# Optimization experiments

Measured on AMD Instinct MI355X. Metric: run time of the kernel, lower is better.

## Reference

```python
import jax, jax.numpy as jnp
import numpy as np

BS, N, H = 8, 2048, 512
NEG_INF = -1.0e9
LEAKY_SLOPE = 0.01  # torch nn.LeakyReLU default


def setup_inputs() -> dict:
    key = jax.random.key(0)
    ks = jax.random.split(key, 8)
    feats = jax.random.normal(ks[0], (BS, N, H), dtype=jnp.float32)
    # random 0/1 adjacency with self-loops so every row has >=1 neighbor
    adj = jax.random.randint(ks[1], (BS, N, N), 0, 2).astype(jnp.float32)
    adj = jnp.maximum(adj, jnp.eye(N, dtype=jnp.float32)[None])
    s = 1.0 / np.sqrt(H)
    return {
        "feats": feats,
        "adj_mat": adj,
        "fc_w": jax.random.normal(ks[2], (H, H), dtype=jnp.float32) * s,
        "fc_b": jax.random.normal(ks[3], (H,), dtype=jnp.float32) * s,
        "q_w": jax.random.normal(ks[4], (1, H), dtype=jnp.float32) * s,
        "q_b": jax.random.normal(ks[5], (1,), dtype=jnp.float32) * s,
        "k_w": jax.random.normal(ks[6], (1, H), dtype=jnp.float32) * s,
        "k_b": jax.random.normal(ks[7], (1,), dtype=jnp.float32) * s,
    }


def reference(feats, adj_mat, fc_w, fc_b, q_w, q_b, k_w, k_b):
    # feats: [bs, N, H]; torch Linear: x @ W.T + b
    feat_proj = jnp.einsum("bnh,oh->bno", feats, fc_w) + fc_b          # [bs, N, H]
    q = jnp.einsum("bnh,oh->bno", feat_proj, q_w) + q_b                # [bs, N, 1]
    k = jnp.einsum("bnh,oh->bno", feat_proj, k_w) + k_b                # [bs, N, 1]
    logits = q + jnp.swapaxes(k, 2, 1)                                 # [bs, N, N] broadcast add
    masked = logits + (1.0 - adj_mat) * NEG_INF
    masked = jnp.where(masked >= 0, masked, LEAKY_SLOPE * masked)      # LeakyReLU
    atten = jax.nn.softmax(masked, axis=-1)
    # dropout is identity in eval mode
    out = jnp.einsum("bnm,bmh->bnh", atten, feat_proj)
    return out + feats  # residual=True
```

## Files before the change

### kernel.cpp

```cpp
#include <hip/hip_runtime.h>
#include <hip/hip_bf16.h>
#include <cstdint>
#include <cstddef>

#define BSZ 8
#define NN 2048
#define HH 512

typedef __attribute__((ext_vector_type(4))) float f32x4;
typedef __attribute__((ext_vector_type(8))) short short8;
typedef __attribute__((ext_vector_type(4))) unsigned short us4;

static __device__ __forceinline__ unsigned short f2bf(float f) {
    uint32_t u = __builtin_bit_cast(uint32_t, f);
    u += 0x7fffu + ((u >> 16) & 1u);
    return (unsigned short)(u >> 16);
}

static __device__ __forceinline__ void async16(const unsigned short* g, unsigned short* l) {
    __builtin_amdgcn_global_load_lds(
        (const __attribute__((address_space(1))) void*)g,
        (__attribute__((address_space(3))) void*)l, 16, 0, 0);
}

__global__ __launch_bounds__(256) void cvt_bf16_k(const float* __restrict__ s,
                                                  unsigned short* __restrict__ d, int n4) {
    int i = blockIdx.x * 256 + threadIdx.x;
    if (i >= n4) return;
    f32x4 v = ((const f32x4*)s)[i];
    us4 o;
    o[0] = f2bf(v[0]); o[1] = f2bf(v[1]); o[2] = f2bf(v[2]); o[3] = f2bf(v[3]);
    ((us4*)d)[i] = o;
}

__global__ __launch_bounds__(256) void eff_w_kernel(
    const float* __restrict__ fc_w, const float* __restrict__ fc_b,
    const float* __restrict__ q_w, const float* __restrict__ q_b,
    const float* __restrict__ k_w, const float* __restrict__ k_b,
    float* __restrict__ wq, float* __restrict__ wk, float* __restrict__ bqk) {
    int h = blockIdx.x * 256 + threadIdx.x;
    float sq = 0.f, sk = 0.f;
    for (int o = 0; o < HH; ++o) {
        float w = fc_w[o * HH + h];
        sq += w * q_w[o];
        sk += w * k_w[o];
    }
    wq[h] = sq; wk[h] = sk;
    if (blockIdx.x == 0) {
        int t = threadIdx.x;
        float bq = fc_b[t] * q_w[t] + fc_b[t + 256] * q_w[t + 256];
        float bk = fc_b[t] * k_w[t] + fc_b[t + 256] * k_w[t + 256];
        for (int off = 32; off; off >>= 1) {
            bq += __shfl_down(bq, off, 64);
            bk += __shfl_down(bk, off, 64);
        }
        __shared__ float rb[8];
        int wv = t >> 6, ln = t & 63;
        if (ln == 0) { rb[wv] = bq; rb[4 + wv] = bk; }
        __syncthreads();
        if (t == 0) bqk[0] = rb[0] + rb[1] + rb[2] + rb[3] + q_b[0];
        if (t == 1) bqk[1] = rb[4] + rb[5] + rb[6] + rb[7] + k_b[0];
    }
}

__global__ __launch_bounds__(256) void qk_kernel(
    const float* __restrict__ feats, const float* __restrict__ wq,
    const float* __restrict__ wk, const float* __restrict__ bqk,
    float* __restrict__ q, float* __restrict__ k) {
    __shared__ float swq[HH], swk[HH];
    const int t = threadIdx.x;
    swq[t] = wq[t]; swq[t + 256] = wq[t + 256];
    swk[t] = wk[t]; swk[t + 256] = wk[t + 256];
    __syncthreads();
    const int wave = t >> 6, lane = t & 63;
    const int row = blockIdx.x * 4 + wave;
    const float* fr = feats + (size_t)row * HH + lane * 8;
    f32x4 v0 = *(const f32x4*)fr;
    f32x4 v1 = *(const f32x4*)(fr + 4);
    const int base = lane * 8;
    float sq = 0.f, sk = 0.f;
#pragma unroll
    for (int c = 0; c < 4; ++c) { sq += v0[c] * swq[base + c];     sk += v0[c] * swk[base + c]; }
#pragma unroll
    for (int c = 0; c < 4; ++c) { sq += v1[c] * swq[base + 4 + c]; sk += v1[c] * swk[base + 4 + c]; }
    for (int off = 32; off; off >>= 1) {
        sq += __shfl_down(sq, off, 64);
        sk += __shfl_down(sk, off, 64);
    }
    if (lane == 0) { q[row] = sq + bqk[0]; k[row] = sk + bqk[1]; }
}

__global__ __launch_bounds__(256) void gemm_fp_kernel(
    const unsigned short* __restrict__ A, const unsigned short* __restrict__ Bt,
    const float* __restrict__ fc_b, unsigned short* __restrict__ fpT) {
    __shared__ alignas(16) unsigned short As[128 * 32];
    __shared__ alignas(16) unsigned short Bs[128 * 32];
    const int tid = threadIdx.x;
    const int wave = tid >> 6, lane = tid & 63;
    const int wi = wave >> 1, wj = wave & 1;
    const int bid = blockIdx.x;
    const int n0 = (bid & 3) * 128;
    const int i0 = (bid >> 2) * 128;
    const int K = HH;
    f32x4 acc[4][4];
#pragma unroll
    for (int a = 0; a < 4; ++a)
#pragma unroll
        for (int b = 0; b < 4; ++b) acc[a][b] = (f32x4)(0.f);

    const int lrow = lane >> 2;
    const int lseg = (lane & 3) * 8;
    const int fro = (lane & 15) * 32 + (lane >> 4) * 8;

    for (int k0 = 0; k0 < K; k0 += 32) {
        __syncthreads();
        {
            const int c0 = wave * 2;
            const unsigned short* ga = A + (size_t)(i0 + c0 * 16 + lrow) * K + k0 + lseg;
            async16(ga, &As[(c0 * 16) * 32]);
            async16(ga + (size_t)16 * K, &As[(c0 * 16 + 16) * 32]);
            const unsigned short* gb = Bt + (size_t)(n0 + c0 * 16 + lrow) * K + k0 + lseg;
            async16(gb, &Bs[(c0 * 16) * 32]);
            async16(gb + (size_t)16 * K, &Bs[(c0 * 16 + 16) * 32]);
        }
        __syncthreads();
        short8 af[4], bf[4];
#pragma unroll
        for (int t = 0; t < 4; ++t) af[t] = *(const short8*)&As[(wi * 64 + t * 16) * 32 + fro];
#pragma unroll
        for (int t = 0; t < 4; ++t) bf[t] = *(const short8*)&Bs[(wj * 64 + t * 16) * 32 + fro];
#pragma unroll
        for (int it = 0; it < 4; ++it)
#pragma unroll
            for (int jt = 0; jt < 4; ++jt)
                acc[it][jt] = __builtin_amdgcn_mfma_f32_16x16x32_bf16(af[it], bf[jt], acc[it][jt], 0, 0, 0);
    }

    const int b = i0 >> 11;
    const int il = i0 & 2047;
#pragma unroll
    for (int jt = 0; jt < 4; ++jt) {
        const int col = n0 + wj * 64 + jt * 16 + (lane & 15);
        const float cb = fc_b[col];
#pragma unroll
        for (int it = 0; it < 4; ++it) {
            const int rb = wi * 64 + it * 16 + ((lane >> 4) << 2);
            us4 o;
#pragma unroll
            for (int r = 0; r < 4; ++r) o[r] = f2bf(acc[it][jt][r] + cb);
            *(us4*)(fpT + ((size_t)b * HH + col) * NN + il + rb) = o;
        }
    }
}

__global__ __launch_bounds__(256) void build_w_kernel(
    const float* __restrict__ adj, const float* __restrict__ q,
    const float* __restrict__ kk, unsigned short* __restrict__ Wd,
    float* __restrict__ rZ) {
    const int row = blockIdx.x;
    const int b = row >> 11;
    const float qi = q[row];
    const float* arow = adj + (size_t)row * NN;
    const float* krow = kk + (b << 11);
    unsigned short* wrow = Wd + (size_t)row * NN;
    const int t = threadIdx.x;
    float z = 0.f;
#pragma unroll
    for (int rep = 0; rep < 2; ++rep) {
        const int j = rep * 1024 + t * 4;
        f32x4 a = *(const f32x4*)(arow + j);
        f32x4 kv = *(const f32x4*)(krow + j);
        us4 o;
#pragma unroll
        for (int c = 0; c < 4; ++c) {
            float s = qi + kv[c];
            s = (s >= 0.f) ? s : 0.01f * s;
            float wv = a[c] * __expf(s);
            z += wv;
            o[c] = f2bf(wv);
        }
        *(us4*)(wrow + j) = o;
    }
    for (int off = 32; off; off >>= 1) z += __shfl_down(z, off, 64);
    __shared__ float zr[4];
    if ((t & 63) == 0) zr[t >> 6] = z;
    __syncthreads();
    if (t == 0) rZ[row] = 1.0f / (zr[0] + zr[1] + zr[2] + zr[3]);
}

__global__ __launch_bounds__(256) void gemm_out_kernel(
    const unsigned short* __restrict__ Wd, const unsigned short* __restrict__ fpT,
    const float* __restrict__ rZ, const float* __restrict__ feats,
    float* __restrict__ out) {
    __shared__ alignas(16) unsigned short As[128 * 32];
    __shared__ alignas(16) unsigned short Bs[128 * 32];
    const int tid = threadIdx.x;
    const int wave = tid >> 6, lane = tid & 63;
    const int wi = wave >> 1, wj = wave & 1;
    const int bid = blockIdx.x;
    const int b = bid & 7;
    const int t6 = bid >> 3;
    const int i0 = (t6 >> 2) * 128;
    const int n0 = (t6 & 3) * 128;
    const int K = NN;
    const unsigned short* A = Wd + (size_t)b * NN * NN;
    const unsigned short* Bt = fpT + (size_t)b * HH * NN;

    f32x4 acc[4][4];
#pragma unroll
    for (int a = 0; a < 4; ++a)
#pragma unroll
        for (int c = 0; c < 4; ++c) acc[a][c] = (f32x4)(0.f);

    const int lrow = lane >> 2;
    const int lseg = (lane & 3) * 8;
    const int fro = (lane & 15) * 32 + (lane >> 4) * 8;

    for (int k0 = 0; k0 < K; k0 += 32) {
        __syncthreads();
        {
            const int c0 = wave * 2;
            const unsigned short* ga = A + (size_t)(i0 + c0 * 16 + lrow) * K + k0 + lseg;
            async16(ga, &As[(c0 * 16) * 32]);
            async16(ga + (size_t)16 * K, &As[(c0 * 16 + 16) * 32]);
            const unsigned short* gb = Bt + (size_t)(n0 + c0 * 16 + lrow) * K + k0 + lseg;
            async16(gb, &Bs[(c0 * 16) * 32]);
            async16(gb + (size_t)16 * K, &Bs[(c0 * 16 + 16) * 32]);
        }
        __syncthreads();
        short8 af[4], bf[4];
#pragma unroll
        for (int t = 0; t < 4; ++t) af[t] = *(const short8*)&As[(wi * 64 + t * 16) * 32 + fro];
#pragma unroll
        for (int t = 0; t < 4; ++t) bf[t] = *(const short8*)&Bs[(wj * 64 + t * 16) * 32 + fro];
#pragma unroll
        for (int it = 0; it < 4; ++it)
#pragma unroll
            for (int jt = 0; jt < 4; ++jt)
                acc[it][jt] = __builtin_amdgcn_mfma_f32_16x16x32_bf16(af[it], bf[jt], acc[it][jt], 0, 0, 0);
    }

#pragma unroll
    for (int it = 0; it < 4; ++it) {
        const int rb = i0 + wi * 64 + it * 16 + ((lane >> 4) << 2);
        f32x4 rz4 = *(const f32x4*)(rZ + (b << 11) + rb);
#pragma unroll
        for (int jt = 0; jt < 4; ++jt) {
            const int col = n0 + wj * 64 + jt * 16 + (lane & 15);
#pragma unroll
            for (int r = 0; r < 4; ++r) {
                const size_t idx = ((size_t)(b << 11) + rb + r) * HH + col;
                out[idx] = acc[it][jt][r] * rz4[r] + feats[idx];
            }
        }
    }
}

extern "C" void kernel_launch(void* const* d_in, const int* in_sizes, int n_in,
                              void* d_out, int out_size, void* d_ws, size_t ws_size,
                              hipStream_t stream) {
    const float* feats = (const float*)d_in[0];
    const float* adj   = (const float*)d_in[1];
    const float* fc_w  = (const float*)d_in[2];
    const float* fc_b  = (const float*)d_in[3];
    const float* q_w   = (const float*)d_in[4];
    const float* q_b   = (const float*)d_in[5];
    const float* k_w   = (const float*)d_in[6];
    const float* k_b   = (const float*)d_in[7];
    float* out = (float*)d_out;

    char* w = (char*)d_ws;
    auto alloc = [&](size_t bytes) {
        char* p = w;
        w += (bytes + 255) & ~(size_t)255;
        return p;
    };
    unsigned short* feats_bf = (unsigned short*)alloc((size_t)BSZ * NN * HH * 2);
    unsigned short* fcw_bf   = (unsigned short*)alloc((size_t)HH * HH * 2);
    float* wq  = (float*)alloc(HH * 4);
    float* wk  = (float*)alloc(HH * 4);
    float* bqk = (float*)alloc(256);
    float* qv  = (float*)alloc((size_t)BSZ * NN * 4);
    float* kv  = (float*)alloc((size_t)BSZ * NN * 4);
    float* rZ  = (float*)alloc((size_t)BSZ * NN * 4);
    unsigned short* fpT = (unsigned short*)alloc((size_t)BSZ * HH * NN * 2);
    unsigned short* Wd  = (unsigned short*)alloc((size_t)BSZ * NN * NN * 2);

    cvt_bf16_k<<<(BSZ * NN * HH / 4 + 255) / 256, 256, 0, stream>>>(feats, feats_bf, BSZ * NN * HH / 4);
    cvt_bf16_k<<<(HH * HH / 4 + 255) / 256, 256, 0, stream>>>(fc_w, fcw_bf, HH * HH / 4);
    eff_w_kernel<<<2, 256, 0, stream>>>(fc_w, fc_b, q_w, q_b, k_w, k_b, wq, wk, bqk);
    qk_kernel<<<BSZ * NN / 4, 256, 0, stream>>>(feats, wq, wk, bqk, qv, kv);
    gemm_fp_kernel<<<(BSZ * NN / 128) * (HH / 128), 256, 0, stream>>>(feats_bf, fcw_bf, fc_b, fpT);
    build_w_kernel<<<BSZ * NN, 256, 0, stream>>>(adj, qv, kv, Wd, rZ);
    gemm_out_kernel<<<BSZ * (NN / 128) * (HH / 128), 256, 0, stream>>>(Wd, fpT, rZ, feats, out);
}
```

Baseline: 366.6 us.

## Merge prep kernels, co-schedule projection GEMM with weight build, split-K output GEMM

The bf16 conversion of feats is fused with the q/k dot products in one prep kernel, and the fc_w conversion runs in extra blocks of that same kernel. A single launch now holds the feature-projection GEMM, the adjacency-weight build and a copy of feats into out, so these independent stages can overlap. The output GEMM is split in two halves along K (256 to 512 blocks) for more parallelism, and each half adds its partial result into out with unsafe float atomics instead of adding the residual. This removes several launches and re-reads of feats, but atomic accumulation makes the float sum order nondeterministic and adds read-modify-write traffic on out.

```diff
diff --git a/kernel.cpp b/kernel.cpp
--- a/kernel.cpp
+++ b/kernel.cpp
@@ -10,6 +10,7 @@
 typedef __attribute__((ext_vector_type(4))) float f32x4;
 typedef __attribute__((ext_vector_type(8))) short short8;
 typedef __attribute__((ext_vector_type(4))) unsigned short us4;
+typedef __attribute__((ext_vector_type(8))) unsigned short us8;
 
 static __device__ __forceinline__ unsigned short f2bf(float f) {
     uint32_t u = __builtin_bit_cast(uint32_t, f);
@@ -21,16 +22,6 @@
     __builtin_amdgcn_global_load_lds(
         (const __attribute__((address_space(1))) void*)g,
         (__attribute__((address_space(3))) void*)l, 16, 0, 0);
-}
-
-__global__ __launch_bounds__(256) void cvt_bf16_k(const float* __restrict__ s,
-                                                  unsigned short* __restrict__ d, int n4) {
-    int i = blockIdx.x * 256 + threadIdx.x;
-    if (i >= n4) return;
-    f32x4 v = ((const f32x4*)s)[i];
-    us4 o;
-    o[0] = f2bf(v[0]); o[1] = f2bf(v[1]); o[2] = f2bf(v[2]); o[3] = f2bf(v[3]);
-    ((us4*)d)[i] = o;
 }
 
 __global__ __launch_bounds__(256) void eff_w_kernel(
@@ -63,56 +54,188 @@
     }
 }
 
-__global__ __launch_bounds__(256) void qk_kernel(
-    const float* __restrict__ feats, const float* __restrict__ wq,
-    const float* __restrict__ wk, const float* __restrict__ bqk,
-    float* __restrict__ q, float* __restrict__ k) {
-    __shared__ float swq[HH], swk[HH];
+__global__ __launch_bounds__(256) void prep_kernel(
+    const float* __restrict__ feats, const float* __restrict__ fc_w,
+    const float* __restrict__ wq, const float* __restrict__ wk,
+    const float* __restrict__ bqk,
+    unsigned short* __restrict__ feats_bf, unsigned short* __restrict__ fcw_bf,
+    float* __restrict__ qv, float* __restrict__ kv) {
+    const int bid = blockIdx.x;
     const int t = threadIdx.x;
-    swq[t] = wq[t]; swq[t + 256] = wq[t + 256];
-    swk[t] = wk[t]; swk[t + 256] = wk[t + 256];
-    __syncthreads();
-    const int wave = t >> 6, lane = t & 63;
-    const int row = blockIdx.x * 4 + wave;
-    const float* fr = feats + (size_t)row * HH + lane * 8;
-    f32x4 v0 = *(const f32x4*)fr;
-    f32x4 v1 = *(const f32x4*)(fr + 4);
-    const int base = lane * 8;
-    float sq = 0.f, sk = 0.f;
-#pragma unroll
-    for (int c = 0; c < 4; ++c) { sq += v0[c] * swq[base + c];     sk += v0[c] * swk[base + c]; }
-#pragma unroll
-    for (int c = 0; c < 4; ++c) { sq += v1[c] * swq[base + 4 + c]; sk += v1[c] * swk[base + 4 + c]; }
-    for (int off = 32; off; off >>= 1) {
-        sq += __shfl_down(sq, off, 64);
-        sk += __shfl_down(sk, off, 64);
-    }
-    if (lane == 0) { q[row] = sq + bqk[0]; k[row] = sk + bqk[1]; }
-}
-
-__global__ __launch_bounds__(256) void gemm_fp_kernel(
+    if (bid < 4096) {
+        __shared__ float swq[HH], swk[HH];
+        swq[t] = wq[t]; swq[t + 256] = wq[t + 256];
+        swk[t] = wk[t]; swk[t + 256] = wk[t + 256];
+        __syncthreads();
+        const int wave = t >> 6, lane = t & 63;
+        const int row = bid * 4 + wave;
+        const float* fr = feats + (size_t)row * HH + lane * 8;
+        f32x4 v0 = *(const f32x4*)fr;
+        f32x4 v1 = *(const f32x4*)(fr + 4);
+        us8 o;
+#pragma unroll
+        for (int c = 0; c < 4; ++c) { o[c] = f2bf(v0[c]); o[4 + c] = f2bf(v1[c]); }
+        *(us8*)(feats_bf + (size_t)row * HH + lane * 8) = o;
+        const int base = lane * 8;
+        float sq = 0.f, sk = 0.f;
+#pragma unroll
+        for (int c = 0; c < 4; ++c) { sq += v0[c] * swq[base + c];     sk += v0[c] * swk[base + c]; }
+#pragma unroll
+        for (int c = 0; c < 4; ++c) { sq += v1[c] * swq[base + 4 + c]; sk += v1[c] * swk[base + 4 + c]; }
+        for (int off = 32; off; off >>= 1) {
+            sq += __shfl_down(sq, off, 64);
+            sk += __shfl_down(sk, off, 64);
+        }
+        if (lane == 0) { qv[row] = sq + bqk[0]; kv[row] = sk + bqk[1]; }
+    } else {
+        const int c = bid - 4096;
+        const int base = c * 1024 + t;
+#pragma unroll
+        for (int j = 0; j < 4; ++j) {
+            const int i = base + j * 256;
+            f32x4 v = ((const f32x4*)fc_w)[i];
+            us4 o;
+#pragma unroll
+            for (int cc = 0; cc < 4; ++cc) o[cc] = f2bf(v[cc]);
+            ((us4*)fcw_bf)[i] = o;
+        }
+    }
+}
+
+__global__ __launch_bounds__(256) void mega_kernel(
     const unsigned short* __restrict__ A, const unsigned short* __restrict__ Bt,
-    const float* __restrict__ fc_b, unsigned short* __restrict__ fpT) {
+    const float* __restrict__ fc_b, unsigned short* __restrict__ fpT,
+    const float* __restrict__ adj, const float* __restrict__ qv,
+    const float* __restrict__ kvv, unsigned short* __restrict__ Wd,
+    float* __restrict__ rZ, const float* __restrict__ feats,
+    float* __restrict__ out) {
+    const int bid = blockIdx.x;
+    const int tid = threadIdx.x;
+    if (bid < 512) {
+        __shared__ alignas(16) unsigned short As[128 * 32];
+        __shared__ alignas(16) unsigned short Bs[128 * 32];
+        const int wave = tid >> 6, lane = tid & 63;
+        const int wi = wave >> 1, wj = wave & 1;
+        const int n0 = (bid & 3) * 128;
+        const int i0 = (bid >> 2) * 128;
+        const int K = HH;
+        f32x4 acc[4][4];
+#pragma unroll
+        for (int a = 0; a < 4; ++a)
+#pragma unroll
+            for (int b = 0; b < 4; ++b) acc[a][b] = (f32x4)(0.f);
+        const int lrow = lane >> 2;
+        const int lseg = (lane & 3) * 8;
+        const int fro = (lane & 15) * 32 + (lane >> 4) * 8;
+        for (int k0 = 0; k0 < K; k0 += 32) {
+            __syncthreads();
+            {
+                const int c0 = wave * 2;
+                const unsigned short* ga = A + (size_t)(i0 + c0 * 16 + lrow) * K + k0 + lseg;
+                async16(ga, &As[(c0 * 16) * 32]);
+                async16(ga + (size_t)16 * K, &As[(c0 * 16 + 16) * 32]);
+                const unsigned short* gb = Bt + (size_t)(n0 + c0 * 16 + lrow) * K + k0 + lseg;
+                async16(gb, &Bs[(c0 * 16) * 32]);
+                async16(gb + (size_t)16 * K, &Bs[(c0 * 16 + 16) * 32]);
+            }
+            __syncthreads();
+            short8 af[4], bf[4];
+#pragma unroll
+            for (int tt = 0; tt < 4; ++tt) af[tt] = *(const short8*)&As[(wi * 64 + tt * 16) * 32 + fro];
+#pragma unroll
+            for (int tt = 0; tt < 4; ++tt) bf[tt] = *(const short8*)&Bs[(wj * 64 + tt * 16) * 32 + fro];
+#pragma unroll
+            for (int it = 0; it < 4; ++it)
+#pragma unroll
+                for (int jt = 0; jt < 4; ++jt)
+                    acc[it][jt] = __builtin_amdgcn_mfma_f32_16x16x32_bf16(af[it], bf[jt], acc[it][jt], 0, 0, 0);
+        }
+        const int b = i0 >> 11;
+        const int il = i0 & 2047;
+#pragma unroll
+        for (int jt = 0; jt < 4; ++jt) {
+            const int col = n0 + wj * 64 + jt * 16 + (lane & 15);
+            const float cb = fc_b[col];
+#pragma unroll
+            for (int it = 0; it < 4; ++it) {
+                const int rb = wi * 64 + it * 16 + ((lane >> 4) << 2);
+                us4 o;
+#pragma unroll
+                for (int r = 0; r < 4; ++r) o[r] = f2bf(acc[it][jt][r] + cb);
+                *(us4*)(fpT + ((size_t)b * HH + col) * NN + il + rb) = o;
+            }
+        }
+    } else if (bid < 512 + 16384) {
+        const int row = bid - 512;
+        const int b = row >> 11;
+        const float qi = qv[row];
+        const float* arow = adj + (size_t)row * NN;
+        const float* krow = kvv + (b << 11);
+        unsigned short* wrow = Wd + (size_t)row * NN;
+        float z = 0.f;
+#pragma unroll
+        for (int rep = 0; rep < 2; ++rep) {
+            const int j = rep * 1024 + tid * 4;
+            f32x4 a = *(const f32x4*)(arow + j);
+            f32x4 kk = *(const f32x4*)(krow + j);
+            us4 o;
+#pragma unroll
+            for (int c = 0; c < 4; ++c) {
+                float s = qi + kk[c];
+                s = (s >= 0.f) ? s : 0.01f * s;
+                float wv = a[c] * __expf(s);
+                z += wv;
+                o[c] = f2bf(wv);
+            }
+            *(us4*)(wrow + j) = o;
+        }
+        for (int off = 32; off; off >>= 1) z += __shfl_down(z, off, 64);
+        __shared__ float zr[4];
+        if ((tid & 63) == 0) zr[tid >> 6] = z;
+        __syncthreads();
+        if (tid == 0) rZ[row] = 1.0f / (zr[0] + zr[1] + zr[2] + zr[3]);
+    } else {
+        const int c = bid - 16896;
+        const int base = c * 1024 + tid;
+#pragma unroll
+        for (int j = 0; j < 4; ++j) {
+            const int i = base + j * 256;
+            ((f32x4*)out)[i] = ((const f32x4*)feats)[i];
+        }
+    }
+}
+
+__global__ __launch_bounds__(256) void gemm_out_kernel(
+    const unsigned short* __restrict__ Wd, const unsigned short* __restrict__ fpT,
+    const float* __restrict__ rZ, float* __restrict__ out) {
     __shared__ alignas(16) unsigned short As[128 * 32];
     __shared__ alignas(16) unsigned short Bs[128 * 32];
     const int tid = threadIdx.x;
     const int wave = tid >> 6, lane = tid & 63;
     const int wi = wave >> 1, wj = wave & 1;
     const int bid = blockIdx.x;
-    const int n0 = (bid & 3) * 128;
-    const int i0 = (bid >> 2) * 128;
-    const int K = HH;
+    const int b = bid & 7;
+    const int r8 = bid >> 3;
+    const int kh = r8 & 1;
+    const int t6 = r8 >> 1;
+    const int i0 = (t6 >> 2) * 128;
+    const int n0 = (t6 & 3) * 128;
+    const int K = NN;
+    const unsigned short* A = Wd + (size_t)b * NN * NN;
+    const unsigned short* Bt = fpT + (size_t)b * HH * NN;
+
     f32x4 acc[4][4];
 #pragma unroll
     for (int a = 0; a < 4; ++a)
 #pragma unroll
-        for (int b = 0; b < 4; ++b) acc[a][b] = (f32x4)(0.f);
+        for (int c = 0; c < 4; ++c) acc[a][c] = (f32x4)(0.f);
 
     const int lrow = lane >> 2;
     const int lseg = (lane & 3) * 8;
     const int fro = (lane & 15) * 32 + (lane >> 4) * 8;
 
-    for (int k0 = 0; k0 < K; k0 += 32) {
+    const int kbeg = kh << 10;
+    for (int k0 = kbeg; k0 < kbeg + 1024; k0 += 32) {
         __syncthreads();
         {
             const int c0 = wave * 2;
@@ -136,110 +259,6 @@
                 acc[it][jt] = __builtin_amdgcn_mfma_f32_16x16x32_bf16(af[it], bf[jt], acc[it][jt], 0, 0, 0);
     }
 
-    const int b = i0 >> 11;
-    const int il = i0 & 2047;
-#pragma unroll
-    for (int jt = 0; jt < 4; ++jt) {
-        const int col = n0 + wj * 64 + jt * 16 + (lane & 15);
-        const float cb = fc_b[col];
-#pragma unroll
-        for (int it = 0; it < 4; ++it) {
-            const int rb = wi * 64 + it * 16 + ((lane >> 4) << 2);
-            us4 o;
-#pragma unroll
-            for (int r = 0; r < 4; ++r) o[r] = f2bf(acc[it][jt][r] + cb);
-            *(us4*)(fpT + ((size_t)b * HH + col) * NN + il + rb) = o;
-        }
-    }
-}
-
-__global__ __launch_bounds__(256) void build_w_kernel(
-    const float* __restrict__ adj, const float* __restrict__ q,
-    const float* __restrict__ kk, unsigned short* __restrict__ Wd,
-    float* __restrict__ rZ) {
-    const int row = blockIdx.x;
-    const int b = row >> 11;
-    const float qi = q[row];
-    const float* arow = adj + (size_t)row * NN;
-    const float* krow = kk + (b << 11);
-    unsigned short* wrow = Wd + (size_t)row * NN;
-    const int t = threadIdx.x;
-    float z = 0.f;
-#pragma unroll
-    for (int rep = 0; rep < 2; ++rep) {
-        const int j = rep * 1024 + t * 4;
-        f32x4 a = *(const f32x4*)(arow + j);
-        f32x4 kv = *(const f32x4*)(krow + j);
-        us4 o;
-#pragma unroll
-        for (int c = 0; c < 4; ++c) {
-            float s = qi + kv[c];
-            s = (s >= 0.f) ? s : 0.01f * s;
-            float wv = a[c] * __expf(s);
-            z += wv;
-            o[c] = f2bf(wv);
-        }
-        *(us4*)(wrow + j) = o;
-    }
-    for (int off = 32; off; off >>= 1) z += __shfl_down(z, off, 64);
-    __shared__ float zr[4];
-    if ((t & 63) == 0) zr[t >> 6] = z;
-    __syncthreads();
-    if (t == 0) rZ[row] = 1.0f / (zr[0] + zr[1] + zr[2] + zr[3]);
-}
-
-__global__ __launch_bounds__(256) void gemm_out_kernel(
-    const unsigned short* __restrict__ Wd, const unsigned short* __restrict__ fpT,
-    const float* __restrict__ rZ, const float* __restrict__ feats,
-    float* __restrict__ out) {
-    __shared__ alignas(16) unsigned short As[128 * 32];
-    __shared__ alignas(16) unsigned short Bs[128 * 32];
-    const int tid = threadIdx.x;
-    const int wave = tid >> 6, lane = tid & 63;
-    const int wi = wave >> 1, wj = wave & 1;
-    const int bid = blockIdx.x;
-    const int b = bid & 7;
-    const int t6 = bid >> 3;
-    const int i0 = (t6 >> 2) * 128;
-    const int n0 = (t6 & 3) * 128;
-    const int K = NN;
-    const unsigned short* A = Wd + (size_t)b * NN * NN;
-    const unsigned short* Bt = fpT + (size_t)b * HH * NN;
-
-    f32x4 acc[4][4];
-#pragma unroll
-    for (int a = 0; a < 4; ++a)
-#pragma unroll
-        for (int c = 0; c < 4; ++c) acc[a][c] = (f32x4)(0.f);
-
-    const int lrow = lane >> 2;
-    const int lseg = (lane & 3) * 8;
-    const int fro = (lane & 15) * 32 + (lane >> 4) * 8;
-
-    for (int k0 = 0; k0 < K; k0 += 32) {
-        __syncthreads();
-        {
-            const int c0 = wave * 2;
-            const unsigned short* ga = A + (size_t)(i0 + c0 * 16 + lrow) * K + k0 + lseg;
-            async16(ga, &As[(c0 * 16) * 32]);
-            async16(ga + (size_t)16 * K, &As[(c0 * 16 + 16) * 32]);
-            const unsigned short* gb = Bt + (size_t)(n0 + c0 * 16 + lrow) * K + k0 + lseg;
-            async16(gb, &Bs[(c0 * 16) * 32]);
-            async16(gb + (size_t)16 * K, &Bs[(c0 * 16 + 16) * 32]);
-        }
-        __syncthreads();
-        short8 af[4], bf[4];
-#pragma unroll
-        for (int t = 0; t < 4; ++t) af[t] = *(const short8*)&As[(wi * 64 + t * 16) * 32 + fro];
-#pragma unroll
-        for (int t = 0; t < 4; ++t) bf[t] = *(const short8*)&Bs[(wj * 64 + t * 16) * 32 + fro];
-#pragma unroll
-        for (int it = 0; it < 4; ++it)
-#pragma unroll
-            for (int jt = 0; jt < 4; ++jt)
-                acc[it][jt] = __builtin_amdgcn_mfma_f32_16x16x32_bf16(af[it], bf[jt], acc[it][jt], 0, 0, 0);
-    }
-
 #pragma unroll
     for (int it = 0; it < 4; ++it) {
         const int rb = i0 + wi * 64 + it * 16 + ((lane >> 4) << 2);
@@ -250,7 +269,7 @@
 #pragma unroll
             for (int r = 0; r < 4; ++r) {
                 const size_t idx = ((size_t)(b << 11) + rb + r) * HH + col;
-                out[idx] = acc[it][jt][r] * rz4[r] + feats[idx];
+                unsafeAtomicAdd(&out[idx], acc[it][jt][r] * rz4[r]);
             }
         }
     }
@@ -286,11 +305,10 @@
     unsigned short* fpT = (unsigned short*)alloc((size_t)BSZ * HH * NN * 2);
     unsigned short* Wd  = (unsigned short*)alloc((size_t)BSZ * NN * NN * 2);
 
-    cvt_bf16_k<<<(BSZ * NN * HH / 4 + 255) / 256, 256, 0, stream>>>(feats, feats_bf, BSZ * NN * HH / 4);
-    cvt_bf16_k<<<(HH * HH / 4 + 255) / 256, 256, 0, stream>>>(fc_w, fcw_bf, HH * HH / 4);
     eff_w_kernel<<<2, 256, 0, stream>>>(fc_w, fc_b, q_w, q_b, k_w, k_b, wq, wk, bqk);
-    qk_kernel<<<BSZ * NN / 4, 256, 0, stream>>>(feats, wq, wk, bqk, qv, kv);
-    gemm_fp_kernel<<<(BSZ * NN / 128) * (HH / 128), 256, 0, stream>>>(feats_bf, fcw_bf, fc_b, fpT);
-    build_w_kernel<<<BSZ * NN, 256, 0, stream>>>(adj, qv, kv, Wd, rZ);
-    gemm_out_kernel<<<BSZ * (NN / 128) * (HH / 128), 256, 0, stream>>>(Wd, fpT, rZ, feats, out);
-}
+    prep_kernel<<<4096 + 64, 256, 0, stream>>>(feats, fc_w, wq, wk, bqk,
+                                               feats_bf, fcw_bf, qv, kv);
+    mega_kernel<<<512 + 16384 + 2048, 256, 0, stream>>>(feats_bf, fcw_bf, fc_b, fpT,
+                                                        adj, qv, kv, Wd, rZ, feats, out);
+    gemm_out_kernel<<<BSZ * (NN / 128) * (HH / 128) * 2, 256, 0, stream>>>(Wd, fpT, rZ, out);
+}
```

After: 400.3 us. 9.2% more time.

## Fuse attention weight build into PV GEMM and pack adjacency into bitmask

Applied to the files above, without the earlier changes.

Collapses seven launches into two. The first kernel converts fp32 to bf16 inside the projection GEMM, takes q/k partials from the GEMM epilogue, and in extra blocks packs the adjacency matrix into a bitmask. The second kernel builds the exp-weighted mask tile on the fly in LDS, accumulates the softmax denominators and runs the PV GEMM. This removes the large bf16 weight matrix write and read and the separate conversion passes. In exchange the exp work is recomputed across the four column tiles, and q/k now come from bf16-rounded GEMM outputs rather than fp32 values.

```diff
diff --git a/kernel.cpp b/kernel.cpp
--- a/kernel.cpp
+++ b/kernel.cpp
@@ -6,6 +6,7 @@
 #define BSZ 8
 #define NN 2048
 #define HH 512
+#define MROWS (BSZ * NN)
 
 typedef __attribute__((ext_vector_type(4))) float f32x4;
 typedef __attribute__((ext_vector_type(8))) short short8;
@@ -23,177 +24,135 @@
         (__attribute__((address_space(3))) void*)l, 16, 0, 0);
 }
 
-__global__ __launch_bounds__(256) void cvt_bf16_k(const float* __restrict__ s,
-                                                  unsigned short* __restrict__ d, int n4) {
-    int i = blockIdx.x * 256 + threadIdx.x;
-    if (i >= n4) return;
-    f32x4 v = ((const f32x4*)s)[i];
-    us4 o;
-    o[0] = f2bf(v[0]); o[1] = f2bf(v[1]); o[2] = f2bf(v[2]); o[3] = f2bf(v[3]);
-    ((us4*)d)[i] = o;
-}
-
-__global__ __launch_bounds__(256) void eff_w_kernel(
-    const float* __restrict__ fc_w, const float* __restrict__ fc_b,
-    const float* __restrict__ q_w, const float* __restrict__ q_b,
-    const float* __restrict__ k_w, const float* __restrict__ k_b,
-    float* __restrict__ wq, float* __restrict__ wk, float* __restrict__ bqk) {
-    int h = blockIdx.x * 256 + threadIdx.x;
-    float sq = 0.f, sk = 0.f;
-    for (int o = 0; o < HH; ++o) {
-        float w = fc_w[o * HH + h];
-        sq += w * q_w[o];
-        sk += w * k_w[o];
-    }
-    wq[h] = sq; wk[h] = sk;
-    if (blockIdx.x == 0) {
-        int t = threadIdx.x;
-        float bq = fc_b[t] * q_w[t] + fc_b[t + 256] * q_w[t + 256];
-        float bk = fc_b[t] * k_w[t] + fc_b[t + 256] * k_w[t + 256];
-        for (int off = 32; off; off >>= 1) {
-            bq += __shfl_down(bq, off, 64);
-            bk += __shfl_down(bk, off, 64);
-        }
-        __shared__ float rb[8];
-        int wv = t >> 6, ln = t & 63;
-        if (ln == 0) { rb[wv] = bq; rb[4 + wv] = bk; }
+__global__ __launch_bounds__(256) void k1_kernel(
+    const float* __restrict__ feats, const float* __restrict__ fc_w,
+    const float* __restrict__ fc_b, const float* __restrict__ q_w,
+    const float* __restrict__ k_w, const float* __restrict__ adj,
+    unsigned short* __restrict__ fpT, unsigned char* __restrict__ maskb,
+    float* __restrict__ qpart, float* __restrict__ kpart) {
+    const int bid = blockIdx.x;
+    const int tid = threadIdx.x;
+    if (bid < 512) {
+        __shared__ alignas(16) unsigned short As[128 * 32];
+        __shared__ alignas(16) unsigned short Bs[128 * 32];
+        __shared__ float qred[2][128], kred[2][128];
+        const int wave = tid >> 6, lane = tid & 63;
+        const int wi = wave >> 1, wj = wave & 1;
+        const int n0 = (bid & 3) * 128;
+        const int i0 = (bid >> 2) * 128;
+        const int r0 = tid >> 3;
+        const int c4 = (tid & 7) * 4;
+        const int fro = (lane & 15) * 32 + (lane >> 4) * 8;
+        f32x4 acc[4][4];
+#pragma unroll
+        for (int a = 0; a < 4; ++a)
+#pragma unroll
+            for (int c = 0; c < 4; ++c) acc[a][c] = (f32x4)(0.f);
+
+        for (int k0 = 0; k0 < HH; k0 += 32) {
+            __syncthreads();
+#pragma unroll
+            for (int m = 0; m < 4; ++m) {
+                f32x4 av = *(const f32x4*)&feats[(size_t)(i0 + r0 + 32 * m) * HH + k0 + c4];
+                f32x4 bv = *(const f32x4*)&fc_w[(size_t)(n0 + r0 + 32 * m) * HH + k0 + c4];
+                us4 oa, ob;
+#pragma unroll
+                for (int c = 0; c < 4; ++c) { oa[c] = f2bf(av[c]); ob[c] = f2bf(bv[c]); }
+                *(us4*)&As[(r0 + 32 * m) * 32 + c4] = oa;
+                *(us4*)&Bs[(r0 + 32 * m) * 32 + c4] = ob;
+            }
+            __syncthreads();
+            short8 af[4], bf[4];
+#pragma unroll
+            for (int t = 0; t < 4; ++t) af[t] = *(const short8*)&As[(wi * 64 + t * 16) * 32 + fro];
+#pragma unroll
+            for (int t = 0; t < 4; ++t) bf[t] = *(const short8*)&Bs[(wj * 64 + t * 16) * 32 + fro];
+#pragma unroll
+            for (int it = 0; it < 4; ++it)
+#pragma unroll
+                for (int jt = 0; jt < 4; ++jt)
+                    acc[it][jt] = __builtin_amdgcn_mfma_f32_16x16x32_bf16(af[it], bf[jt], acc[it][jt], 0, 0, 0);
+        }
+
+        int colv[4]; float cbv[4], qwv[4], kwv[4];
+#pragma unroll
+        for (int jt = 0; jt < 4; ++jt) {
+            colv[jt] = n0 + wj * 64 + jt * 16 + (lane & 15);
+            cbv[jt] = fc_b[colv[jt]];
+            qwv[jt] = q_w[colv[jt]];
+            kwv[jt] = k_w[colv[jt]];
+        }
+        const int b = i0 >> 11;
+        const int il = i0 & 2047;
+#pragma unroll
+        for (int jt = 0; jt < 4; ++jt) {
+#pragma unroll
+            for (int it = 0; it < 4; ++it) {
+                const int rb = wi * 64 + it * 16 + ((lane >> 4) << 2);
+                us4 o;
+#pragma unroll
+                for (int r = 0; r < 4; ++r) o[r] = f2bf(acc[it][jt][r] + cbv[jt]);
+                *(us4*)(fpT + ((size_t)b * HH + colv[jt]) * NN + il + rb) = o;
+            }
+        }
+#pragma unroll
+        for (int it = 0; it < 4; ++it) {
+#pragma unroll
+            for (int r = 0; r < 4; ++r) {
+                float pq = 0.f, pk = 0.f;
+#pragma unroll
+                for (int jt = 0; jt < 4; ++jt) {
+                    float v = acc[it][jt][r] + cbv[jt];
+                    pq += v * qwv[jt];
+                    pk += v * kwv[jt];
+                }
+                for (int off = 1; off < 16; off <<= 1) {
+                    pq += __shfl_xor(pq, off, 64);
+                    pk += __shfl_xor(pk, off, 64);
+                }
+                if ((lane & 15) == 0) {
+                    const int rr = wi * 64 + it * 16 + ((lane >> 4) << 2) + r;
+                    qred[wj][rr] = pq;
+                    kred[wj][rr] = pk;
+                }
+            }
+        }
         __syncthreads();
-        if (t == 0) bqk[0] = rb[0] + rb[1] + rb[2] + rb[3] + q_b[0];
-        if (t == 1) bqk[1] = rb[4] + rb[5] + rb[6] + rb[7] + k_b[0];
-    }
-}
-
-__global__ __launch_bounds__(256) void qk_kernel(
-    const float* __restrict__ feats, const float* __restrict__ wq,
-    const float* __restrict__ wk, const float* __restrict__ bqk,
-    float* __restrict__ q, float* __restrict__ k) {
-    __shared__ float swq[HH], swk[HH];
-    const int t = threadIdx.x;
-    swq[t] = wq[t]; swq[t + 256] = wq[t + 256];
-    swk[t] = wk[t]; swk[t + 256] = wk[t + 256];
-    __syncthreads();
-    const int wave = t >> 6, lane = t & 63;
-    const int row = blockIdx.x * 4 + wave;
-    const float* fr = feats + (size_t)row * HH + lane * 8;
-    f32x4 v0 = *(const f32x4*)fr;
-    f32x4 v1 = *(const f32x4*)(fr + 4);
-    const int base = lane * 8;
-    float sq = 0.f, sk = 0.f;
-#pragma unroll
-    for (int c = 0; c < 4; ++c) { sq += v0[c] * swq[base + c];     sk += v0[c] * swk[base + c]; }
-#pragma unroll
-    for (int c = 0; c < 4; ++c) { sq += v1[c] * swq[base + 4 + c]; sk += v1[c] * swk[base + 4 + c]; }
-    for (int off = 32; off; off >>= 1) {
-        sq += __shfl_down(sq, off, 64);
-        sk += __shfl_down(sk, off, 64);
-    }
-    if (lane == 0) { q[row] = sq + bqk[0]; k[row] = sk + bqk[1]; }
-}
-
-__global__ __launch_bounds__(256) void gemm_fp_kernel(
-    const unsigned short* __restrict__ A, const unsigned short* __restrict__ Bt,
-    const float* __restrict__ fc_b, unsigned short* __restrict__ fpT) {
+        if (tid < 128) {
+            const size_t o = (size_t)(n0 >> 7) * MROWS + i0 + tid;
+            qpart[o] = qred[0][tid] + qred[1][tid];
+            kpart[o] = kred[0][tid] + kred[1][tid];
+        }
+    } else {
+        const int a = bid - 512;
+        const int wave = tid >> 6, lane = tid & 63;
+#pragma unroll
+        for (int s = 0; s < 4; ++s) {
+            const int row = a * 16 + s * 4 + wave;
+            const float* ar = adj + (size_t)row * NN;
+#pragma unroll
+            for (int p = 0; p < 4; ++p) {
+                f32x4 v0 = *(const f32x4*)&ar[p * 512 + lane * 8];
+                f32x4 v1 = *(const f32x4*)&ar[p * 512 + lane * 8 + 4];
+                float fb = v0[0] + 2.f * v0[1] + 4.f * v0[2] + 8.f * v0[3]
+                         + 16.f * v1[0] + 32.f * v1[1] + 64.f * v1[2] + 128.f * v1[3];
+                maskb[(size_t)row * 256 + p * 64 + lane] = (unsigned char)(unsigned int)fb;
+            }
+        }
+    }
+}
+
+__global__ __launch_bounds__(256) void fused_pv_kernel(
+    const unsigned short* __restrict__ fpT, const unsigned char* __restrict__ maskb,
+    const float* __restrict__ qpart, const float* __restrict__ kpart,
+    const float* __restrict__ q_b, const float* __restrict__ k_b,
+    const float* __restrict__ feats, float* __restrict__ out) {
     __shared__ alignas(16) unsigned short As[128 * 32];
     __shared__ alignas(16) unsigned short Bs[128 * 32];
-    const int tid = threadIdx.x;
-    const int wave = tid >> 6, lane = tid & 63;
-    const int wi = wave >> 1, wj = wave & 1;
-    const int bid = blockIdx.x;
-    const int n0 = (bid & 3) * 128;
-    const int i0 = (bid >> 2) * 128;
-    const int K = HH;
-    f32x4 acc[4][4];
-#pragma unroll
-    for (int a = 0; a < 4; ++a)
-#pragma unroll
-        for (int b = 0; b < 4; ++b) acc[a][b] = (f32x4)(0.f);
-
-    const int lrow = lane >> 2;
-    const int lseg = (lane & 3) * 8;
-    const int fro = (lane & 15) * 32 + (lane >> 4) * 8;
-
-    for (int k0 = 0; k0 < K; k0 += 32) {
-        __syncthreads();
-        {
-            const int c0 = wave * 2;
-            const unsigned short* ga = A + (size_t)(i0 + c0 * 16 + lrow) * K + k0 + lseg;
-            async16(ga, &As[(c0 * 16) * 32]);
-            async16(ga + (size_t)16 * K, &As[(c0 * 16 + 16) * 32]);
-            const unsigned short* gb = Bt + (size_t)(n0 + c0 * 16 + lrow) * K + k0 + lseg;
-            async16(gb, &Bs[(c0 * 16) * 32]);
-            async16(gb + (size_t)16 * K, &Bs[(c0 * 16 + 16) * 32]);
-        }
-        __syncthreads();
-        short8 af[4], bf[4];
-#pragma unroll
-        for (int t = 0; t < 4; ++t) af[t] = *(const short8*)&As[(wi * 64 + t * 16) * 32 + fro];
-#pragma unroll
-        for (int t = 0; t < 4; ++t) bf[t] = *(const short8*)&Bs[(wj * 64 + t * 16) * 32 + fro];
-#pragma unroll
-        for (int it = 0; it < 4; ++it)
-#pragma unroll
-            for (int jt = 0; jt < 4; ++jt)
-                acc[it][jt] = __builtin_amdgcn_mfma_f32_16x16x32_bf16(af[it], bf[jt], acc[it][jt], 0, 0, 0);
-    }
-
-    const int b = i0 >> 11;
-    const int il = i0 & 2047;
-#pragma unroll
-    for (int jt = 0; jt < 4; ++jt) {
-        const int col = n0 + wj * 64 + jt * 16 + (lane & 15);
-        const float cb = fc_b[col];
-#pragma unroll
-        for (int it = 0; it < 4; ++it) {
-            const int rb = wi * 64 + it * 16 + ((lane >> 4) << 2);
-            us4 o;
-#pragma unroll
-            for (int r = 0; r < 4; ++r) o[r] = f2bf(acc[it][jt][r] + cb);
-            *(us4*)(fpT + ((size_t)b * HH + col) * NN + il + rb) = o;
-        }
-    }
-}
-
-__global__ __launch_bounds__(256) void build_w_kernel(
-    const float* __restrict__ adj, const float* __restrict__ q,
-    const float* __restrict__ kk, unsigned short* __restrict__ Wd,
-    float* __restrict__ rZ) {
-    const int row = blockIdx.x;
-    const int b = row >> 11;
-    const float qi = q[row];
-    const float* arow = adj + (size_t)row * NN;
-    const float* krow = kk + (b << 11);
-    unsigned short* wrow = Wd + (size_t)row * NN;
-    const int t = threadIdx.x;
-    float z = 0.f;
-#pragma unroll
-    for (int rep = 0; rep < 2; ++rep) {
-        const int j = rep * 1024 + t * 4;
-        f32x4 a = *(const f32x4*)(arow + j);
-        f32x4 kv = *(const f32x4*)(krow + j);
-        us4 o;
-#pragma unroll
-        for (int c = 0; c < 4; ++c) {
-            float s = qi + kv[c];
-            s = (s >= 0.f) ? s : 0.01f * s;
-            float wv = a[c] * __expf(s);
-            z += wv;
-            o[c] = f2bf(wv);
-        }
-        *(us4*)(wrow + j) = o;
-    }
-    for (int off = 32; off; off >>= 1) z += __shfl_down(z, off, 64);
-    __shared__ float zr[4];
-    if ((t & 63) == 0) zr[t >> 6] = z;
-    __syncthreads();
-    if (t == 0) rZ[row] = 1.0f / (zr[0] + zr[1] + zr[2] + zr[3]);
-}
-
-__global__ __launch_bounds__(256) void gemm_out_kernel(
-    const unsigned short* __restrict__ Wd, const unsigned short* __restrict__ fpT,
-    const float* __restrict__ rZ, const float* __restrict__ feats,
-    float* __restrict__ out) {
-    __shared__ alignas(16) unsigned short As[128 * 32];
-    __shared__ alignas(16) unsigned short Bs[128 * 32];
+    __shared__ float kLDS[NN];
+    __shared__ float qLDS[128];
+    __shared__ float zbuf[4][32][8];
+    __shared__ float rzl[128];
     const int tid = threadIdx.x;
     const int wave = tid >> 6, lane = tid & 63;
     const int wi = wave >> 1, wj = wave & 1;
@@ -202,9 +161,36 @@
     const int t6 = bid >> 3;
     const int i0 = (t6 >> 2) * 128;
     const int n0 = (t6 & 3) * 128;
-    const int K = NN;
-    const unsigned short* A = Wd + (size_t)b * NN * NN;
+    const size_t rowbase = (size_t)b * NN + i0;
+
+    {
+        const float kb = k_b[0], qb = q_b[0];
+#pragma unroll
+        for (int s = 0; s < 8; ++s) {
+            const int j = s * 256 + tid;
+            const size_t gj = (size_t)b * NN + j;
+            kLDS[j] = qpart[0] * 0.f + kpart[gj] + kpart[MROWS + gj]
+                    + kpart[2 * MROWS + gj] + kpart[3 * MROWS + gj] + kb;
+        }
+        if (tid < 128) {
+            const size_t gi = rowbase + tid;
+            qLDS[tid] = qpart[gi] + qpart[MROWS + gi]
+                      + qpart[2 * MROWS + gi] + qpart[3 * MROWS + gi] + qb;
+        }
+    }
+    __syncthreads();
+
+    const int r0 = tid >> 3;
+    const int c4 = (tid & 7) * 4;
+    float qi[4];
+#pragma unroll
+    for (int m = 0; m < 4; ++m) qi[m] = qLDS[r0 + 32 * m];
+    float z[4] = {0.f, 0.f, 0.f, 0.f};
+
     const unsigned short* Bt = fpT + (size_t)b * HH * NN;
+    const uint32_t* mk = (const uint32_t*)maskb;
+    const int lrow = lane >> 2, lseg = (lane & 3) * 8;
+    const int fro = (lane & 15) * 32 + (lane >> 4) * 8;
 
     f32x4 acc[4][4];
 #pragma unroll
@@ -212,20 +198,39 @@
 #pragma unroll
         for (int c = 0; c < 4; ++c) acc[a][c] = (f32x4)(0.f);
 
-    const int lrow = lane >> 2;
-    const int lseg = (lane & 3) * 8;
-    const int fro = (lane & 15) * 32 + (lane >> 4) * 8;
-
-    for (int k0 = 0; k0 < K; k0 += 32) {
+    uint32_t mcur[4];
+#pragma unroll
+    for (int m = 0; m < 4; ++m) mcur[m] = mk[(rowbase + r0 + 32 * m) * 64];
+
+    for (int k0 = 0; k0 < NN; k0 += 32) {
         __syncthreads();
         {
             const int c0 = wave * 2;
-            const unsigned short* ga = A + (size_t)(i0 + c0 * 16 + lrow) * K + k0 + lseg;
-            async16(ga, &As[(c0 * 16) * 32]);
-            async16(ga + (size_t)16 * K, &As[(c0 * 16 + 16) * 32]);
-            const unsigned short* gb = Bt + (size_t)(n0 + c0 * 16 + lrow) * K + k0 + lseg;
+            const unsigned short* gb = Bt + (size_t)(n0 + c0 * 16 + lrow) * NN + k0 + lseg;
             async16(gb, &Bs[(c0 * 16) * 32]);
-            async16(gb + (size_t)16 * K, &Bs[(c0 * 16 + 16) * 32]);
+            async16(gb + (size_t)16 * NN, &Bs[(c0 * 16 + 16) * 32]);
+        }
+        uint32_t mnext[4];
+        if (k0 + 32 < NN) {
+#pragma unroll
+            for (int m = 0; m < 4; ++m)
+                mnext[m] = mk[(rowbase + r0 + 32 * m) * 64 + ((k0 + 32) >> 5)];
+        }
+        const f32x4 kv = *(const f32x4*)&kLDS[k0 + c4];
+#pragma unroll
+        for (int m = 0; m < 4; ++m) {
+            const uint32_t nib = (mcur[m] >> c4) & 0xFu;
+            us4 o;
+#pragma unroll
+            for (int c = 0; c < 4; ++c) {
+                float s = qi[m] + kv[c];
+                s = (s >= 0.f) ? s : 0.01f * s;
+                const float e = __expf(s);
+                const float wv = ((nib >> c) & 1u) ? e : 0.f;
+                z[m] += wv;
+                o[c] = f2bf(wv);
+            }
+            *(us4*)&As[(r0 + 32 * m) * 32 + c4] = o;
         }
         __syncthreads();
         short8 af[4], bf[4];
@@ -238,19 +243,35 @@
 #pragma unroll
             for (int jt = 0; jt < 4; ++jt)
                 acc[it][jt] = __builtin_amdgcn_mfma_f32_16x16x32_bf16(af[it], bf[jt], acc[it][jt], 0, 0, 0);
-    }
+#pragma unroll
+        for (int m = 0; m < 4; ++m) mcur[m] = mnext[m];
+    }
+
+#pragma unroll
+    for (int m = 0; m < 4; ++m) zbuf[m][r0][tid & 7] = z[m];
+    __syncthreads();
+    if (tid < 128) {
+        float s = 0.f;
+        const float* zp = zbuf[tid >> 5][tid & 31];
+#pragma unroll
+        for (int j = 0; j < 8; ++j) s += zp[j];
+        rzl[tid] = 1.0f / s;
+    }
+    __syncthreads();
 
 #pragma unroll
     for (int it = 0; it < 4; ++it) {
-        const int rb = i0 + wi * 64 + it * 16 + ((lane >> 4) << 2);
-        f32x4 rz4 = *(const f32x4*)(rZ + (b << 11) + rb);
+        const int rb = wi * 64 + it * 16 + ((lane >> 4) << 2);
+        float rv[4];
+#pragma unroll
+        for (int r = 0; r < 4; ++r) rv[r] = rzl[rb + r];
 #pragma unroll
         for (int jt = 0; jt < 4; ++jt) {
             const int col = n0 + wj * 64 + jt * 16 + (lane & 15);
 #pragma unroll
             for (int r = 0; r < 4; ++r) {
-                const size_t idx = ((size_t)(b << 11) + rb + r) * HH + col;
-                out[idx] = acc[it][jt][r] * rz4[r] + feats[idx];
+                const size_t idx = (rowbase + rb + r) * HH + col;
+                out[idx] = acc[it][jt][r] * rv[r] + feats[idx];
             }
         }
     }
@@ -275,22 +296,13 @@
         w += (bytes + 255) & ~(size_t)255;
         return p;
     };
-    unsigned short* feats_bf = (unsigned short*)alloc((size_t)BSZ * NN * HH * 2);
-    unsigned short* fcw_bf   = (unsigned short*)alloc((size_t)HH * HH * 2);
-    float* wq  = (float*)alloc(HH * 4);
-    float* wk  = (float*)alloc(HH * 4);
-    float* bqk = (float*)alloc(256);
-    float* qv  = (float*)alloc((size_t)BSZ * NN * 4);
-    float* kv  = (float*)alloc((size_t)BSZ * NN * 4);
-    float* rZ  = (float*)alloc((size_t)BSZ * NN * 4);
-    unsigned short* fpT = (unsigned short*)alloc((size_t)BSZ * HH * NN * 2);
-    unsigned short* Wd  = (unsigned short*)alloc((size_t)BSZ * NN * NN * 2);
-
-    cvt_bf16_k<<<(BSZ * NN * HH / 4 + 255) / 256, 256, 0, stream>>>(feats, feats_bf, BSZ * NN * HH / 4);
-    cvt_bf16_k<<<(HH * HH / 4 + 255) / 256, 256, 0, stream>>>(fc_w, fcw_bf, HH * HH / 4);
-    eff_w_kernel<<<2, 256, 0, stream>>>(fc_w, fc_b, q_w, q_b, k_w, k_b, wq, wk, bqk);
-    qk_kernel<<<BSZ * NN / 4, 256, 0, stream>>>(feats, wq, wk, bqk, qv, kv);
-    gemm_fp_kernel<<<(BSZ * NN / 128) * (HH / 128), 256, 0, stream>>>(feats_bf, fcw_bf, fc_b, fpT);
-    build_w_kernel<<<BSZ * NN, 256, 0, stream>>>(adj, qv, kv, Wd, rZ);
-    gemm_out_kernel<<<BSZ * (NN / 128) * (HH / 128), 256, 0, stream>>>(Wd, fpT, rZ, feats, out);
-}
+    unsigned short* fpT   = (unsigned short*)alloc((size_t)BSZ * HH * NN * 2);
+    unsigned char*  maskb = (unsigned char*)alloc((size_t)MROWS * 256);
+    float* qpart = (float*)alloc((size_t)4 * MROWS * 4);
+    float* kpart = (float*)alloc((size_t)4 * MROWS * 4);
+
+    k1_kernel<<<512 + 1024, 256, 0, stream>>>(feats, fc_w, fc_b, q_w, k_w, adj,
+                                              fpT, maskb, qpart, kpart);
+    fused_pv_kernel<<<BSZ * (NN / 128) * (HH / 128), 256, 0, stream>>>(
+        fpT, maskb, qpart, kpart, q_b, k_b, feats, out);
+}
```

After: 337.4 us. 8.0% less time.
